# Optimization experiments

Measured on AMD Instinct MI355X. Metric: run time of the kernel, lower is better.

The kernel has to match this reference:

```python
import jax, jax.numpy as jnp
import numpy as np

N = 16384
IN_FEATS = 128
HIDDEN = 128
OUT_FEATS = 64


def setup_inputs() -> dict:
    key = jax.random.key(0)
    ks = jax.random.split(key, 8)
    x = jax.random.normal(ks[0], (N, IN_FEATS), dtype=jnp.float32)
    adj = jax.random.uniform(ks[1], (N, N), dtype=jnp.float32)
    def glorot(k, shape):
        lim = 1.0 / np.sqrt(shape[0])
        return jax.random.uniform(k, shape, minval=-lim, maxval=lim, dtype=jnp.float32)
    W1 = glorot(ks[2], (IN_FEATS, HIDDEN))
    b1 = jnp.zeros((HIDDEN,), dtype=jnp.float32)
    W2 = glorot(ks[3], (HIDDEN, OUT_FEATS))
    b2 = jnp.zeros((OUT_FEATS,), dtype=jnp.float32)
    W_out = glorot(ks[4], (OUT_FEATS, 1))
    b_out = jnp.zeros((1,), dtype=jnp.float32)
    return {"x": x, "adj": adj, "W1": W1, "b1": b1, "W2": W2, "b2": b2,
            "W_out": W_out, "b_out": b_out}


def _gcn_layer(x, adj, W, b):
    # support = x @ W ; out = adj @ support + b  (standard GraphConvLayer)
    return adj @ (x @ W) + b


def reference(x, adj, W1, b1, W2, b2, W_out, b_out):
    h = jax.nn.relu(_gcn_layer(x, adj, W1, b1))      # [N, hidden]
    h = _gcn_layer(h, adj, W2, b2)                   # [N, out_feats]
    pooled = h.sum(axis=0)                           # [out_feats] graph readout
    return pooled @ W_out + b_out                    # [1]
```

## Files before the change

### kernel.cpp

```cpp
#include <hip/hip_runtime.h>
#include <hip/hip_bf16.h>
#include <stdint.h>

#define NN   16384
#define FI   128
#define FH   128
#define FO   64

#define BM   16
#define BK   64
#define LDK  72
#define NT   (NN / BK)
#define NBLK (NN / BM)
#define NPART NBLK

typedef float f32x4 __attribute__((ext_vector_type(4)));
typedef short s16x8 __attribute__((ext_vector_type(8)));
typedef short s16x4 __attribute__((ext_vector_type(4)));

__device__ __forceinline__ unsigned short f2bf(float f) {
    union { float f; unsigned u; } v; v.f = f;
    unsigned u = v.u;
    return (unsigned short)((u + 0x7FFFu + ((u >> 16) & 1u)) >> 16);
}

__global__ __launch_bounds__(256) void k1_s1t(const float* __restrict__ x,
                                              const float* __restrict__ W1,
                                              unsigned short* __restrict__ S1T) {
    __shared__ float w1s[FI][FH];
    __shared__ float xs[64][132];

    const int t  = threadIdx.x;
    const int b  = blockIdx.x;
    const int k0 = b * 64;

    float* wflat = &w1s[0][0];
    for (int i = t; i < FI * FH; i += 256) wflat[i] = W1[i];

    #pragma unroll
    for (int s = 0; s < 8; ++s) {
        int idx = t + 256 * s;
        int r   = idx >> 5;
        int f4  = idx & 31;
        f32x4 vv = *(const f32x4*)(x + (size_t)(k0 + r) * FI + f4 * 4);
        *(f32x4*)(&xs[r][f4 * 4]) = vv;
    }
    __syncthreads();

    const int w = t >> 6;
    const int l = t & 63;

    float acc[32];
    #pragma unroll
    for (int j = 0; j < 32; ++j) acc[j] = 0.f;

    for (int f4 = 0; f4 < 32; ++f4) {
        f32x4 xv = *(const f32x4*)(&xs[l][f4 * 4]);
        #pragma unroll
        for (int e = 0; e < 4; ++e) {
            const int f = f4 * 4 + e;
            #pragma unroll
            for (int cth = 0; cth < 8; ++cth) {
                f32x4 wv = *(const f32x4*)(&w1s[f][w * 32 + cth * 4]);
                acc[cth * 4 + 0] += xv[e] * wv[0];
                acc[cth * 4 + 1] += xv[e] * wv[1];
                acc[cth * 4 + 2] += xv[e] * wv[2];
                acc[cth * 4 + 3] += xv[e] * wv[3];
            }
        }
    }

    const int k = k0 + l;
    #pragma unroll
    for (int j = 0; j < 32; ++j) {
        const int n = w * 32 + j;
        S1T[(size_t)n * NN + k] = f2bf(acc[j]);
    }
}

__global__ __launch_bounds__(256, 4) void k2_agg(const float* __restrict__ adj,
                                                 const unsigned short* __restrict__ S1T,
                                                 float* __restrict__ T,
                                                 float* __restrict__ cpart) {
    __shared__ unsigned short aA[2][BM][LDK];
    __shared__ float cs[2][4][BK];

    const int  t    = threadIdx.x;
    const long m0   = (long)blockIdx.x * BM;
    const int  w    = t >> 6;
    const int  l    = t & 63;
    const int  ar   = t >> 4;
    const int  ac4  = t & 15;
    const int  m    = l & 15;
    const int  quad = l >> 4;

    f32x4 acc[2];
    acc[0] = (f32x4){0.f, 0.f, 0.f, 0.f};
    acc[1] = (f32x4){0.f, 0.f, 0.f, 0.f};

    f32x4 paA, paB;
    s16x8 bfA[2][2], bfB[2][2];

#define SYNC() do {                                                               \
    asm volatile("s_waitcnt lgkmcnt(0)" ::: "memory");                            \
    __builtin_amdgcn_s_barrier();                                                 \
} while (0)

#define LOADA(PA, KT)                                                             \
    PA = *(const f32x4*)(adj + (m0 + ar) * NN + (long)(KT) * BK + ac4 * 4)

#define LOADB(BF, KT) do {                                                        \
    const long ko_ = (long)(KT) * BK;                                             \
    _Pragma("unroll")                                                             \
    for (int nt_ = 0; nt_ < 2; ++nt_)                                             \
        _Pragma("unroll")                                                         \
        for (int ks_ = 0; ks_ < 2; ++ks_)                                         \
            BF[nt_][ks_] = *(const s16x8*)(                                       \
                S1T + (size_t)(w * 32 + nt_ * 16 + m) * NN + ko_ + ks_ * 32 + quad * 8); \
} while (0)

#define STAGE(SB, PA) do {                                                        \
    s16x4 q_;                                                                     \
    _Pragma("unroll")                                                             \
    for (int j_ = 0; j_ < 4; ++j_) q_[j_] = (short)f2bf(PA[j_]);                  \
    *(s16x4*)(&aA[SB][ar][ac4 * 4]) = q_;                                         \
       \
    f32x4 pv_;                                                                    \
    _Pragma("unroll")                                                             \
    for (int j_ = 0; j_ < 4; ++j_) {                                              \
        float p_ = PA[j_];                                                        \
        p_ += __shfl_xor(p_, 16);                                                 \
        p_ += __shfl_xor(p_, 32);                                                 \
        pv_[j_] = p_;                                                             \
    }                                                                             \
    if (l < 16) *(f32x4*)(&cs[SB][w][l * 4]) = pv_;                               \
} while (0)

#define FLUSH(SB, KCOL) do {                                                      \
    if (t < BK)                                                                   \
        cpart[(size_t)blockIdx.x * NN + (KCOL) + t] =                             \
            cs[SB][0][t] + cs[SB][1][t] + cs[SB][2][t] + cs[SB][3][t];            \
} while (0)

#define COMPUTE(SB, BF) do {                                                      \
    _Pragma("unroll")                                                             \
    for (int ks = 0; ks < 2; ++ks) {                                              \
        s16x8 af_ = *(const s16x8*)(&aA[SB][m][ks * 32 + quad * 8]);              \
        _Pragma("unroll")                                                         \
        for (int nt = 0; nt < 2; ++nt)                                            \
            acc[nt] = __builtin_amdgcn_mfma_f32_16x16x32_bf16(                    \
                af_, BF[nt][ks], acc[nt], 0, 0, 0);                               \
    }                                                                             \
} while (0)

    LOADA(paA, 0);
    LOADA(paB, 1);
    LOADB(bfA, 0);
    LOADB(bfB, 1);
    STAGE(0, paA);
    SYNC();

    for (int kt2 = 0; kt2 < NT; kt2 += 2) {
        if (kt2 + 2 < NT) LOADA(paA, kt2 + 2);
        FLUSH(0, kt2 * BK);
        COMPUTE(0, bfA);
        if (kt2 + 2 < NT) LOADB(bfA, kt2 + 2);
        STAGE(1, paB);
        SYNC();

        if (kt2 + 3 < NT) LOADA(paB, kt2 + 3);
        FLUSH(1, (kt2 + 1) * BK);
        COMPUTE(1, bfB);
        if (kt2 + 3 < NT) LOADB(bfB, kt2 + 3);
        if (kt2 + 2 < NT) STAGE(0, paA);
        SYNC();
    }

#undef LOADA
#undef LOADB
#undef STAGE
#undef FLUSH
#undef COMPUTE
#undef SYNC

    #pragma unroll
    for (int nt = 0; nt < 2; ++nt) {
        const int col = w * 32 + nt * 16 + m;
        #pragma unroll
        for (int r = 0; r < 4; ++r) {
            const long row = m0 + quad * 4 + r;
            T[row * FH + col] = acc[nt][r];
        }
    }
}

__global__ __launch_bounds__(256) void k3_v(const float* __restrict__ T,
                                            const float* __restrict__ cpart,
                                            const float* __restrict__ b1,
                                            float* __restrict__ v) {
    __shared__ float vp[FH];
    __shared__ float cw[4][64];
    __shared__ float cloc[64];

    const int t = threadIdx.x;
    const int b = blockIdx.x;
    const int w = t >> 6;
    const int l = t & 63;

    float s = 0.f;
    #pragma unroll 8
    for (int i = 0; i < NPART / 4; ++i)
        s += cpart[(size_t)(w + 4 * i) * NN + b * 64 + l];
    cw[w][l] = s;
    if (t < FH) vp[t] = 0.f;
    __syncthreads();
    if (t < 64) cloc[t] = cw[0][t] + cw[1][t] + cw[2][t] + cw[3][t];
    __syncthreads();

    const int kk = t >> 2;
    const int mq = t & 3;
    const int k  = b * 64 + kk;
    const float ck = cloc[kk];

    #pragma unroll
    for (int j4 = 0; j4 < 8; ++j4) {
        f32x4 tv = *(const f32x4*)(T + (size_t)k * FH + mq * 32 + j4 * 4);
        f32x4 bv = *(const f32x4*)(b1 + mq * 32 + j4 * 4);
        #pragma unroll
        for (int e = 0; e < 4; ++e) {
            float h = tv[e] + bv[e];
            h = h > 0.f ? h : 0.f;
            atomicAdd(&vp[mq * 32 + j4 * 4 + e], ck * h);
        }
    }
    __syncthreads();
    if (t < FH) atomicAdd(&v[t], vp[t]);
}

__global__ void k4_out(const float* __restrict__ v, const float* __restrict__ W2,
                       const float* __restrict__ b2, const float* __restrict__ Wout,
                       const float* __restrict__ bout, float* __restrict__ out) {
    const int j = threadIdx.x;
    float pj = (float)NN * b2[j];
    for (int mm = 0; mm < FH; ++mm) pj += v[mm] * W2[mm * FO + j];
    float s = pj * Wout[j];
    #pragma unroll
    for (int off = 32; off; off >>= 1) s += __shfl_down(s, off);
    if (j == 0) out[0] = s + bout[0];
}

extern "C" void kernel_launch(void* const* d_in, const int* in_sizes, int n_in,
                              void* d_out, int out_size, void* d_ws, size_t ws_size,
                              hipStream_t stream) {
    const float* x    = (const float*)d_in[0];
    const float* adj  = (const float*)d_in[1];
    const float* W1   = (const float*)d_in[2];
    const float* b1   = (const float*)d_in[3];
    const float* W2   = (const float*)d_in[4];
    const float* b2   = (const float*)d_in[5];
    const float* Wout = (const float*)d_in[6];
    const float* bout = (const float*)d_in[7];
    float* out = (float*)d_out;

    char* ws = (char*)d_ws;
    unsigned short* S1T = (unsigned short*)ws;
    float* T     = (float*)(ws + (4u  << 20));
    float* cpart = (float*)(ws + (12u << 20));
    float* v     = (float*)(ws + (76u << 20));

    hipMemsetAsync(v, 0, 512, stream);

    k1_s1t<<<256, 256, 0, stream>>>(x, W1, S1T);
    k2_agg<<<NBLK, 256, 0, stream>>>(adj, S1T, T, cpart);
    k3_v  <<<256, 256, 0, stream>>>(T, cpart, b1, v);
    k4_out<<<1, 64, 0, stream>>>(v, W2, b2, Wout, bout, out);
}
```

Before: 1.679 ms.

## Restructure adjacency aggregation as split-K, LDS-free per-wave MFMA over all features

The aggregation kernel now gives each wave a 16-row strip across all 128 hidden features and splits the K dimension in half over block pairs. Adjacency values go straight from global memory into MFMA A-fragments with no LDS staging or barriers. Column sums for the later readout are reduced inside each wave and written per wave. The goal is to drop the shared-memory round trip and synchronisation and to raise MFMA work per adj load. In exchange, each K-half writes its own partial T, which k3 must sum, and per-thread register use grows (occupancy hint lowered to 2). Each wave also reloads the S1T fragments independently rather than sharing them.

```diff
diff --git a/kernel.cpp b/kernel.cpp
--- a/kernel.cpp
+++ b/kernel.cpp
@@ -7,16 +7,13 @@
 #define FH   128
 #define FO   64
 
-#define BM   16
-#define BK   64
-#define LDK  72
-#define NT   (NN / BK)
-#define NBLK (NN / BM)
-#define NPART NBLK
+#define KS    32
+#define KHALF (NN / 2)
+#define NS    (KHALF / KS)
+#define NPART 1024
 
 typedef float f32x4 __attribute__((ext_vector_type(4)));
 typedef short s16x8 __attribute__((ext_vector_type(8)));
-typedef short s16x4 __attribute__((ext_vector_type(4)));
 
 __device__ __forceinline__ unsigned short f2bf(float f) {
     union { float f; unsigned u; } v; v.f = f;
@@ -78,123 +75,109 @@
     }
 }
 
-__global__ __launch_bounds__(256, 4) void k2_agg(const float* __restrict__ adj,
+__global__ __launch_bounds__(256, 2) void k2_agg(const float* __restrict__ adj,
                                                  const unsigned short* __restrict__ S1T,
-                                                 float* __restrict__ T,
+                                                 float* __restrict__ Tpart,
                                                  float* __restrict__ cpart) {
-    __shared__ unsigned short aA[2][BM][LDK];
-    __shared__ float cs[2][4][BK];
-
-    const int  t    = threadIdx.x;
-    const long m0   = (long)blockIdx.x * BM;
-    const int  w    = t >> 6;
-    const int  l    = t & 63;
-    const int  ar   = t >> 4;
-    const int  ac4  = t & 15;
-    const int  m    = l & 15;
-    const int  quad = l >> 4;
-
-    f32x4 acc[2];
-    acc[0] = (f32x4){0.f, 0.f, 0.f, 0.f};
-    acc[1] = (f32x4){0.f, 0.f, 0.f, 0.f};
-
-    f32x4 paA, paB;
-    s16x8 bfA[2][2], bfB[2][2];
-
-#define SYNC() do {                                                               \
-    asm volatile("s_waitcnt lgkmcnt(0)" ::: "memory");                            \
-    __builtin_amdgcn_s_barrier();                                                 \
-} while (0)
-
-#define LOADA(PA, KT)                                                             \
-    PA = *(const f32x4*)(adj + (m0 + ar) * NN + (long)(KT) * BK + ac4 * 4)
-
-#define LOADB(BF, KT) do {                                                        \
-    const long ko_ = (long)(KT) * BK;                                             \
-    _Pragma("unroll")                                                             \
-    for (int nt_ = 0; nt_ < 2; ++nt_)                                             \
+    const int t    = threadIdx.x;
+    const int w    = t >> 6;
+    const int l    = t & 63;
+    const int m    = l & 15;
+    const int quad = l >> 4;
+
+    const int rb = blockIdx.x >> 1;
+    const int kh = blockIdx.x & 1;
+    const long r0 = (long)rb * 64 + w * 16;
+    const int  k0 = kh * KHALF;
+
+    f32x4 acc[8];
+    #pragma unroll
+    for (int nt = 0; nt < 8; ++nt) acc[nt] = (f32x4){0.f, 0.f, 0.f, 0.f};
+
+    const float* aptr = adj + (size_t)(r0 + m) * NN + k0 + quad * 8;
+    float* cp = cpart + (size_t)(rb * 4 + w) * NN + k0 + quad * 8;
+
+    f32x4 aC0, aC1, aN0, aN1;
+    s16x8 bC[8], bN[8];
+
+#define LOADA(A0, A1, S) do {                                                     \
+    const float* p_ = aptr + (size_t)(S) * KS;                                    \
+    A0 = *(const f32x4*)p_;                                                       \
+    A1 = *(const f32x4*)(p_ + 4);                                                 \
+} while (0)
+
+#define LOADB(B, S) do {                                                          \
+    const size_t ko_ = (size_t)k0 + (size_t)(S) * KS + quad * 8;                  \
+    _Pragma("unroll")                                                             \
+    for (int nt_ = 0; nt_ < 8; ++nt_)                                             \
+        B[nt_] = *(const s16x8*)(S1T + (size_t)(nt_ * 16 + m) * NN + ko_);        \
+} while (0)
+
+#define CSUM(A0, A1, S) do {                                                      \
+    f32x4 p0_ = A0, p1_ = A1;                                                     \
+    _Pragma("unroll")                                                             \
+    for (int mk_ = 1; mk_ < 16; mk_ <<= 1) {                                      \
         _Pragma("unroll")                                                         \
-        for (int ks_ = 0; ks_ < 2; ++ks_)                                         \
-            BF[nt_][ks_] = *(const s16x8*)(                                       \
-                S1T + (size_t)(w * 32 + nt_ * 16 + m) * NN + ko_ + ks_ * 32 + quad * 8); \
-} while (0)
-
-#define STAGE(SB, PA) do {                                                        \
-    s16x4 q_;                                                                     \
-    _Pragma("unroll")                                                             \
-    for (int j_ = 0; j_ < 4; ++j_) q_[j_] = (short)f2bf(PA[j_]);                  \
-    *(s16x4*)(&aA[SB][ar][ac4 * 4]) = q_;                                         \
-       \
-    f32x4 pv_;                                                                    \
-    _Pragma("unroll")                                                             \
-    for (int j_ = 0; j_ < 4; ++j_) {                                              \
-        float p_ = PA[j_];                                                        \
-        p_ += __shfl_xor(p_, 16);                                                 \
-        p_ += __shfl_xor(p_, 32);                                                 \
-        pv_[j_] = p_;                                                             \
+        for (int e_ = 0; e_ < 4; ++e_) {                                          \
+            p0_[e_] += __shfl_xor(p0_[e_], mk_);                                  \
+            p1_[e_] += __shfl_xor(p1_[e_], mk_);                                  \
+        }                                                                         \
     }                                                                             \
-    if (l < 16) *(f32x4*)(&cs[SB][w][l * 4]) = pv_;                               \
-} while (0)
-
-#define FLUSH(SB, KCOL) do {                                                      \
-    if (t < BK)                                                                   \
-        cpart[(size_t)blockIdx.x * NN + (KCOL) + t] =                             \
-            cs[SB][0][t] + cs[SB][1][t] + cs[SB][2][t] + cs[SB][3][t];            \
-} while (0)
-
-#define COMPUTE(SB, BF) do {                                                      \
-    _Pragma("unroll")                                                             \
-    for (int ks = 0; ks < 2; ++ks) {                                              \
-        s16x8 af_ = *(const s16x8*)(&aA[SB][m][ks * 32 + quad * 8]);              \
-        _Pragma("unroll")                                                         \
-        for (int nt = 0; nt < 2; ++nt)                                            \
-            acc[nt] = __builtin_amdgcn_mfma_f32_16x16x32_bf16(                    \
-                af_, BF[nt][ks], acc[nt], 0, 0, 0);                               \
+    if (m == 0) {                                                                 \
+        float* q_ = cp + (size_t)(S) * KS;                                        \
+        *(f32x4*)q_       = p0_;                                                  \
+        *(f32x4*)(q_ + 4) = p1_;                                                  \
     }                                                                             \
 } while (0)
 
-    LOADA(paA, 0);
-    LOADA(paB, 1);
-    LOADB(bfA, 0);
-    LOADB(bfB, 1);
-    STAGE(0, paA);
-    SYNC();
-
-    for (int kt2 = 0; kt2 < NT; kt2 += 2) {
-        if (kt2 + 2 < NT) LOADA(paA, kt2 + 2);
-        FLUSH(0, kt2 * BK);
-        COMPUTE(0, bfA);
-        if (kt2 + 2 < NT) LOADB(bfA, kt2 + 2);
-        STAGE(1, paB);
-        SYNC();
-
-        if (kt2 + 3 < NT) LOADA(paB, kt2 + 3);
-        FLUSH(1, (kt2 + 1) * BK);
-        COMPUTE(1, bfB);
-        if (kt2 + 3 < NT) LOADB(bfB, kt2 + 3);
-        if (kt2 + 2 < NT) STAGE(0, paA);
-        SYNC();
+#define STEP(A0, A1, B) do {                                                      \
+    s16x8 abf_;                                                                   \
+    _Pragma("unroll")                                                             \
+    for (int e_ = 0; e_ < 4; ++e_) {                                              \
+        abf_[e_]     = (short)f2bf(A0[e_]);                                       \
+        abf_[e_ + 4] = (short)f2bf(A1[e_]);                                       \
+    }                                                                             \
+    _Pragma("unroll")                                                             \
+    for (int nt_ = 0; nt_ < 8; ++nt_)                                             \
+        acc[nt_] = __builtin_amdgcn_mfma_f32_16x16x32_bf16(                       \
+            abf_, B[nt_], acc[nt_], 0, 0, 0);                                     \
+} while (0)
+
+    LOADA(aC0, aC1, 0);
+    LOADB(bC, 0);
+
+    for (int s = 0; s < NS; s += 2) {
+        LOADA(aN0, aN1, s + 1);
+        LOADB(bN, s + 1);
+        CSUM(aC0, aC1, s);
+        STEP(aC0, aC1, bC);
+
+        if (s + 2 < NS) {
+            LOADA(aC0, aC1, s + 2);
+            LOADB(bC, s + 2);
+        }
+        CSUM(aN0, aN1, s + 1);
+        STEP(aN0, aN1, bN);
     }
 
 #undef LOADA
 #undef LOADB
-#undef STAGE
-#undef FLUSH
-#undef COMPUTE
-#undef SYNC
-
-    #pragma unroll
-    for (int nt = 0; nt < 2; ++nt) {
-        const int col = w * 32 + nt * 16 + m;
+#undef CSUM
+#undef STEP
+
+    float* Tp = Tpart + (size_t)kh * NN * FH;
+    #pragma unroll
+    for (int nt = 0; nt < 8; ++nt) {
+        const int col = nt * 16 + m;
         #pragma unroll
         for (int r = 0; r < 4; ++r) {
-            const long row = m0 + quad * 4 + r;
-            T[row * FH + col] = acc[nt][r];
-        }
-    }
-}
-
-__global__ __launch_bounds__(256) void k3_v(const float* __restrict__ T,
+            const long row = r0 + quad * 4 + r;
+            Tp[row * FH + col] = acc[nt][r];
+        }
+    }
+}
+
+__global__ __launch_bounds__(256) void k3_v(const float* __restrict__ Tpart,
                                             const float* __restrict__ cpart,
                                             const float* __restrict__ b1,
                                             float* __restrict__ v) {
@@ -224,11 +207,12 @@
 
     #pragma unroll
     for (int j4 = 0; j4 < 8; ++j4) {
-        f32x4 tv = *(const f32x4*)(T + (size_t)k * FH + mq * 32 + j4 * 4);
+        f32x4 t0 = *(const f32x4*)(Tpart + (size_t)k * FH + mq * 32 + j4 * 4);
+        f32x4 t1 = *(const f32x4*)(Tpart + ((size_t)NN + k) * FH + mq * 32 + j4 * 4);
         f32x4 bv = *(const f32x4*)(b1 + mq * 32 + j4 * 4);
         #pragma unroll
         for (int e = 0; e < 4; ++e) {
-            float h = tv[e] + bv[e];
+            float h = t0[e] + t1[e] + bv[e];
             h = h > 0.f ? h : 0.f;
             atomicAdd(&vp[mq * 32 + j4 * 4 + e], ck * h);
         }
@@ -264,14 +248,14 @@
 
     char* ws = (char*)d_ws;
     unsigned short* S1T = (unsigned short*)ws;
-    float* T     = (float*)(ws + (4u  << 20));
-    float* cpart = (float*)(ws + (12u << 20));
-    float* v     = (float*)(ws + (76u << 20));
+    float* Tpart = (float*)(ws + (4u  << 20));
+    float* cpart = (float*)(ws + (20u << 20));
+    float* v     = (float*)(ws + (84u << 20));
 
     hipMemsetAsync(v, 0, 512, stream);
 
     k1_s1t<<<256, 256, 0, stream>>>(x, W1, S1T);
-    k2_agg<<<NBLK, 256, 0, stream>>>(adj, S1T, T, cpart);
-    k3_v  <<<256, 256, 0, stream>>>(T, cpart, b1, v);
+    k2_agg<<<512, 256, 0, stream>>>(adj, S1T, Tpart, cpart);
+    k3_v  <<<256, 256, 0, stream>>>(Tpart, cpart, b1, v);
     k4_out<<<1, 64, 0, stream>>>(v, W2, b2, Wout, bout, out);
 }
```

Result: slower. 1.835 ms (+9.2%).

## Stage S1T tiles into swizzled LDS via global_load_lds in aggregation kernel

Applied to the files above, without the earlier changes.

The aggregation kernel stops loading the bf16 S1T operand straight into registers. It now uses async global-to-LDS loads (global_load_lds, 16 bytes) into a double-buffered LDS tile with an XOR swizzle to avoid bank conflicts, and MFMA operands are read back from LDS. The main loop changes from a two-step unrolled register ping-pong to a single-step loop synchronised with vmcnt/lgkmcnt waits and barriers. The aim is to cut register pressure and hide global latency. The cost is prefetch depth dropping from two tiles to one, plus extra LDS use and LDS reads.

```diff
diff --git a/kernel.cpp b/kernel.cpp
--- a/kernel.cpp
+++ b/kernel.cpp
@@ -9,7 +9,6 @@
 
 #define BM   16
 #define BK   64
-#define LDK  72
 #define NT   (NN / BK)
 #define NBLK (NN / BM)
 #define NPART NBLK
@@ -22,6 +21,12 @@
     union { float f; unsigned u; } v; v.f = f;
     unsigned u = v.u;
     return (unsigned short)((u + 0x7FFFu + ((u >> 16) & 1u)) >> 16);
+}
+
+__device__ __forceinline__ void gl_lds16(const unsigned short* g, unsigned short* l) {
+    __builtin_amdgcn_global_load_lds(
+        (const __attribute__((address_space(1))) void*)g,
+        (__attribute__((address_space(3))) void*)l, 16, 0, 0);
 }
 
 __global__ __launch_bounds__(256) void k1_s1t(const float* __restrict__ x,
@@ -82,106 +87,103 @@
                                                  const unsigned short* __restrict__ S1T,
                                                  float* __restrict__ T,
                                                  float* __restrict__ cpart) {
-    __shared__ unsigned short aA[2][BM][LDK];
-    __shared__ float cs[2][4][BK];
+    __shared__ __attribute__((aligned(16))) unsigned short aA[2][BM][72];
+    __shared__ __attribute__((aligned(16))) unsigned short bB[2][FH][BK];
+    __shared__ __attribute__((aligned(16))) float cs[2][4][BK];
 
     const int  t    = threadIdx.x;
     const long m0   = (long)blockIdx.x * BM;
     const int  w    = t >> 6;
     const int  l    = t & 63;
-    const int  ar   = t >> 4;
+    const int  arow = t >> 4;
     const int  ac4  = t & 15;
     const int  m    = l & 15;
     const int  quad = l >> 4;
 
+    const int brow = w * 32 + (l >> 3);
+    const int bcol = 8 * ((l & 7) ^ (l >> 3));
+
     f32x4 acc[2];
     acc[0] = (f32x4){0.f, 0.f, 0.f, 0.f};
     acc[1] = (f32x4){0.f, 0.f, 0.f, 0.f};
 
-    f32x4 paA, paB;
-    s16x8 bfA[2][2], bfB[2][2];
-
-#define SYNC() do {                                                               \
-    asm volatile("s_waitcnt lgkmcnt(0)" ::: "memory");                            \
-    __builtin_amdgcn_s_barrier();                                                 \
-} while (0)
-
-#define LOADA(PA, KT)                                                             \
-    PA = *(const f32x4*)(adj + (m0 + ar) * NN + (long)(KT) * BK + ac4 * 4)
-
-#define LOADB(BF, KT) do {                                                        \
-    const long ko_ = (long)(KT) * BK;                                             \
-    _Pragma("unroll")                                                             \
-    for (int nt_ = 0; nt_ < 2; ++nt_)                                             \
-        _Pragma("unroll")                                                         \
-        for (int ks_ = 0; ks_ < 2; ++ks_)                                         \
-            BF[nt_][ks_] = *(const s16x8*)(                                       \
-                S1T + (size_t)(w * 32 + nt_ * 16 + m) * NN + ko_ + ks_ * 32 + quad * 8); \
-} while (0)
-
-#define STAGE(SB, PA) do {                                                        \
-    s16x4 q_;                                                                     \
-    _Pragma("unroll")                                                             \
-    for (int j_ = 0; j_ < 4; ++j_) q_[j_] = (short)f2bf(PA[j_]);                  \
-    *(s16x4*)(&aA[SB][ar][ac4 * 4]) = q_;                                         \
-       \
+    f32x4 pa;
+
+#define LOADA(KT)                                                                 \
+    pa = *(const f32x4*)(adj + (m0 + arow) * NN + (long)(KT) * BK + ac4 * 4)
+
+#define STAGEB(SB, KT) do {                                                       \
+    const size_t ko_ = (size_t)(KT) * BK;                                         \
+    _Pragma("unroll")                                                             \
+    for (int j_ = 0; j_ < 4; ++j_)                                                \
+        gl_lds16(S1T + (size_t)(brow + j_ * 8) * NN + ko_ + bcol,                 \
+                 &bB[SB][w * 32 + j_ * 8][0]);                                    \
+} while (0)
+
+#define STAGEA(SB) do {                                                           \
+                   \
     f32x4 pv_;                                                                    \
     _Pragma("unroll")                                                             \
     for (int j_ = 0; j_ < 4; ++j_) {                                              \
-        float p_ = PA[j_];                                                        \
+        float p_ = pa[j_];                                                        \
         p_ += __shfl_xor(p_, 16);                                                 \
         p_ += __shfl_xor(p_, 32);                                                 \
         pv_[j_] = p_;                                                             \
     }                                                                             \
     if (l < 16) *(f32x4*)(&cs[SB][w][l * 4]) = pv_;                               \
-} while (0)
-
-#define FLUSH(SB, KCOL) do {                                                      \
+    s16x4 q_;                                                                     \
+    _Pragma("unroll")                                                             \
+    for (int j_ = 0; j_ < 4; ++j_) q_[j_] = (short)f2bf(pa[j_]);                  \
+    *(s16x4*)(&aA[SB][arow][ac4 * 4]) = q_;                                       \
+} while (0)
+
+#define FLUSH(SB, KT) do {                                                        \
     if (t < BK)                                                                   \
-        cpart[(size_t)blockIdx.x * NN + (KCOL) + t] =                             \
+        cpart[(size_t)blockIdx.x * NN + (size_t)(KT) * BK + t] =                  \
             cs[SB][0][t] + cs[SB][1][t] + cs[SB][2][t] + cs[SB][3][t];            \
 } while (0)
 
-#define COMPUTE(SB, BF) do {                                                      \
+#define COMPUTE(SB) do {                                                          \
     _Pragma("unroll")                                                             \
     for (int ks = 0; ks < 2; ++ks) {                                              \
-        s16x8 af_ = *(const s16x8*)(&aA[SB][m][ks * 32 + quad * 8]);              \
+        s16x8 af_ = *(const s16x8*)((const char*)&aA[SB][m][0] +                  \
+                                    ks * 64 + quad * 16);                         \
         _Pragma("unroll")                                                         \
-        for (int nt = 0; nt < 2; ++nt)                                            \
+        for (int nt = 0; nt < 2; ++nt) {                                          \
+            const int row_ = w * 32 + nt * 16 + m;                                \
+            s16x8 bf_ = *(const s16x8*)((const char*)&bB[SB][row_][0] +           \
+                          ((ks * 64 + quad * 16) ^ ((m & 7) << 4)));              \
             acc[nt] = __builtin_amdgcn_mfma_f32_16x16x32_bf16(                    \
-                af_, BF[nt][ks], acc[nt], 0, 0, 0);                               \
+                af_, bf_, acc[nt], 0, 0, 0);                                      \
+        }                                                                         \
     }                                                                             \
 } while (0)
 
-    LOADA(paA, 0);
-    LOADA(paB, 1);
-    LOADB(bfA, 0);
-    LOADB(bfB, 1);
-    STAGE(0, paA);
-    SYNC();
-
-    for (int kt2 = 0; kt2 < NT; kt2 += 2) {
-        if (kt2 + 2 < NT) LOADA(paA, kt2 + 2);
-        FLUSH(0, kt2 * BK);
-        COMPUTE(0, bfA);
-        if (kt2 + 2 < NT) LOADB(bfA, kt2 + 2);
-        STAGE(1, paB);
-        SYNC();
-
-        if (kt2 + 3 < NT) LOADA(paB, kt2 + 3);
-        FLUSH(1, (kt2 + 1) * BK);
-        COMPUTE(1, bfB);
-        if (kt2 + 3 < NT) LOADB(bfB, kt2 + 3);
-        if (kt2 + 2 < NT) STAGE(0, paA);
-        SYNC();
+    LOADA(0);
+    STAGEB(0, 0);
+    STAGEA(0);
+    LOADA(1);
+    asm volatile("s_waitcnt vmcnt(1) lgkmcnt(0)" ::: "memory");
+    __builtin_amdgcn_s_barrier();
+
+    for (int kt = 0; kt < NT; ++kt) {
+        const int cur = kt & 1;
+        if (kt + 1 < NT) {
+            STAGEB(cur ^ 1, kt + 1);
+            STAGEA(cur ^ 1);
+            if (kt + 2 < NT) LOADA(kt + 2);
+        }
+        FLUSH(cur, kt);
+        COMPUTE(cur);
+        asm volatile("s_waitcnt vmcnt(1) lgkmcnt(0)" ::: "memory");
+        __builtin_amdgcn_s_barrier();
     }
 
 #undef LOADA
-#undef LOADB
-#undef STAGE
+#undef STAGEB
+#undef STAGEA
 #undef FLUSH
 #undef COMPUTE
-#undef SYNC
 
     #pragma unroll
     for (int nt = 0; nt < 2; ++nt) {
```

Result: faster. 1.596 ms (-4.9%).
